# Performance work log

Hardware: AMD Instinct MI355X
Metric: run time of the kernel (lower is better)

Reference implementation:

```python
import jax, jax.numpy as jnp
import numpy as np

NUM_HEADS = 16
MASKED_BIAS = -10000.0


def setup_inputs() -> dict:
    key = jax.random.key(0)
    k1, k2, k3 = jax.random.split(key, 3)
    B, S, D = 4, 2048, 1024
    return {
        "hidden_states": jax.random.normal(k1, (B, S, D), dtype=jnp.float32),
        "attention_mask": jnp.ones((B, S), dtype=jnp.float32),
        "w_attn": jax.random.normal(k2, (D, 3 * D), dtype=jnp.float32) * 0.02,
        "b_attn": jax.random.normal(k3, (3 * D,), dtype=jnp.float32) * 0.1,
    }


def reference(hidden_states, attention_mask, w_attn, b_attn):
    B, S, D = hidden_states.shape
    H = NUM_HEADS
    Dh = D // H
    # Conv1D: x @ W + b  -> [B, S, 3D]
    qkv = hidden_states @ w_attn + b_attn
    q, k, v = jnp.split(qkv, 3, axis=-1)

    def split_heads(t):  # [B,S,D] -> [B,H,S,Dh]
        return t.reshape(B, S, H, Dh).transpose(0, 2, 1, 3)

    q, k, v = split_heads(q), split_heads(k), split_heads(v)
    present = jnp.stack([k, v], axis=0)  # concat_key_value

    # process_mask: (1 - mask) * -10000, broadcast [B,1,1,S]
    add_mask = (1.0 - attention_mask)[:, None, None, :] * MASKED_BIAS

    qk = jnp.einsum("bhqd,bhkd->bhqk", q, k)
    norm_qk = qk * (1.0 / float(Dh) ** 0.5)
    causal = jnp.tril(jnp.ones((S, S), dtype=bool))[None, None]
    attn_weights = jnp.where(causal, norm_qk, jnp.asarray(MASKED_BIAS, norm_qk.dtype))
    attn_weights = attn_weights + add_mask
    probs = jax.nn.softmax(attn_weights, axis=-1)
    attn_output = jnp.einsum("bhqk,bhkd->bhqd", probs, v)
    # merge heads -> [B,S,D]
    attn_output = attn_output.transpose(0, 2, 1, 3).reshape(B, S, D)
    return attn_output, present
```

## Files before the change

kernel.cpp:

```cpp
#include <hip/hip_runtime.h>
#include <stdint.h>


#define B_SZ    4
#define S_LEN   2048
#define D_MODEL 1024
#define N3      3072
#define H_NUM   16
#define DH      64
#define M_TOT   8192

typedef __attribute__((ext_vector_type(8))) short short8;
typedef __attribute__((ext_vector_type(4))) short bf16x4;
typedef __attribute__((ext_vector_type(4))) float f32x4;

#define LOG2E      1.4426950408889634f
#define SCL2E      0.18033688011112042f
#define MASKB2     (-14426.9504f)

__device__ __forceinline__ unsigned short f2b(float f) {
  union { float f; unsigned int u; } x;
  x.f = f;
  unsigned int u = x.u;
  u += 0x7fffu + ((u >> 16) & 1u);
  return (unsigned short)(u >> 16);
}

__device__ __forceinline__ unsigned int cvt_pk_bf16(float lo, float hi) {
  unsigned int r;
  asm("v_cvt_pk_bf16_f32 %0, %1, %2" : "=v"(r) : "v"(lo), "v"(hi));
  return r;
}

__device__ __forceinline__ float exp2_fast(float x) {
#if __has_builtin(__builtin_amdgcn_exp2f)
  return __builtin_amdgcn_exp2f(x);
#else
  return __expf(x * 0.6931471805599453f);
#endif
}

__device__ __forceinline__ f32x4 mfma16(bf16x4 a, bf16x4 b, f32x4 c) {
#if __has_builtin(__builtin_amdgcn_mfma_f32_16x16x16bf16_1k)
  return __builtin_amdgcn_mfma_f32_16x16x16bf16_1k(a, b, c, 0, 0, 0);
#else
  asm("v_mfma_f32_16x16x16_bf16 %0, %1, %2, %0" : "+v"(c) : "v"(a), "v"(b));
  return c;
#endif
}

__device__ __forceinline__ void async16(const void* g, void* l) {
  __builtin_amdgcn_global_load_lds((const __attribute__((address_space(1))) void*)g,
                                   (__attribute__((address_space(3))) void*)l,
                                   16, 0, 0);
}

__global__ void k_convert_x(const float* __restrict__ X, unsigned short* __restrict__ Xb) {
  const int i = (blockIdx.x * 256 + threadIdx.x) * 4;
  const float4 v = *(const float4*)(X + i);
  ushort4 o;
  o.x = f2b(v.x); o.y = f2b(v.y); o.z = f2b(v.z); o.w = f2b(v.w);
  *(ushort4*)(Xb + i) = o;
}

__global__ void k_wt(const float* __restrict__ W, unsigned short* __restrict__ Wt) {
  __shared__ float tile[32][33];
  const int n0 = blockIdx.x * 32, k0 = blockIdx.y * 32;
  const int tx = threadIdx.x, ty = threadIdx.y;
  for (int i = 0; i < 32; i += 8)
    tile[ty + i][tx] = W[(size_t)(k0 + ty + i) * N3 + n0 + tx];
  __syncthreads();
  for (int i = 0; i < 32; i += 8)
    Wt[(size_t)(n0 + ty + i) * D_MODEL + k0 + tx] = f2b(tile[tx][ty + i]);
}

__global__ __launch_bounds__(256) void k_gemm_qkv(
    const unsigned short* __restrict__ Xb, const unsigned short* __restrict__ Wt,
    const float* __restrict__ bias,
    unsigned short* __restrict__ Qb, unsigned short* __restrict__ Kb,
    float* __restrict__ presK, float* __restrict__ presV) {
  __shared__ __align__(16) unsigned short SMEM[8192];
  unsigned short* As = SMEM;
  unsigned short* Bs = SMEM + 4096;
  const int t = threadIdx.x;
  const int lane = t & 63, wave = t >> 6;
  const int g = lane >> 4, c = lane & 15;
  const int m0 = blockIdx.y * 128, n0 = blockIdx.x * 128;
  const int wm = (wave >> 1) * 64, wn = (wave & 1) * 64;

  const f32x4 zero = {0.f, 0.f, 0.f, 0.f};
  f32x4 acc[4][4];
  for (int i = 0; i < 4; ++i)
    for (int j = 0; j < 4; ++j) acc[i][j] = zero;

  const int row_a = t >> 2;
  const int col_a = (t & 3) * 8;
  const unsigned short* gA = Xb + (size_t)(m0 + row_a) * D_MODEL + col_a;
  const unsigned short* gB = Wt + (size_t)(n0 + row_a) * D_MODEL + col_a;
  const int wbase = wave * 1024;

  for (int k0 = 0; k0 < D_MODEL; k0 += 32) {
    __syncthreads();
    async16(gA + k0,                (char*)As + wbase);
    async16(gA + k0 + 64 * D_MODEL, (char*)As + 4096 + wbase);
    async16(gB + k0,                (char*)Bs + wbase);
    async16(gB + k0 + 64 * D_MODEL, (char*)Bs + 4096 + wbase);
    __syncthreads();

    short8 af[4], bf[4];
    for (int mi = 0; mi < 4; ++mi)
      af[mi] = *(const short8*)(As + (wm + mi * 16 + c) * 32 + g * 8);
    for (int ni = 0; ni < 4; ++ni)
      bf[ni] = *(const short8*)(Bs + (wn + ni * 16 + c) * 32 + g * 8);
    for (int mi = 0; mi < 4; ++mi)
      for (int ni = 0; ni < 4; ++ni)
        acc[mi][ni] = __builtin_amdgcn_mfma_f32_16x16x32_bf16(af[mi], bf[ni], acc[mi][ni], 0, 0, 0);
  }

  __syncthreads();

  const int sec = (n0 + wn) >> 10;
  const int h = ((n0 + wn) & 1023) >> 6;
  unsigned short* slab = SMEM + wave * 1152;
  float bv[4];
  for (int ni = 0; ni < 4; ++ni) bv[ni] = bias[n0 + wn + ni * 16 + c];

  for (int mi = 0; mi < 4; ++mi) {
    const int mrow = m0 + wm + mi * 16;

    if (sec != 2) {
      for (int ni = 0; ni < 4; ++ni)
        for (int r = 0; r < 4; ++r)
          slab[(g * 4 + r) * 72 + ni * 16 + c] = f2b(acc[mi][ni][r] + bv[ni]);
      const short8 w0 = *(const short8*)(slab + c * 72 + g * 16);
      const short8 w1 = *(const short8*)(slab + c * 72 + g * 16 + 8);
      const int srow = mrow + c;
      const int b = srow >> 11, s = srow & 2047;
      unsigned short* dst = (sec == 0 ? Qb : Kb) +
          ((size_t)((b * H_NUM + h) * S_LEN + s)) * DH + g * 16;
      *(short8*)(dst) = w0;
      *(short8*)(dst + 8) = w1;
    }
    if (sec >= 1) {
      float* dstf = (sec == 1) ? presK : presV;
      for (int ni = 0; ni < 4; ++ni) {
        const int dh = ni * 16 + c;
        for (int r = 0; r < 4; ++r) {
          const int m = mrow + g * 4 + r;
          const int b = m >> 11, s = m & 2047;
          dstf[((size_t)((b * H_NUM + h) * S_LEN + s)) * DH + dh] =
              acc[mi][ni][r] + bv[ni];
        }
      }
    }
  }
}

__global__ __launch_bounds__(256) void k_vt(const float* __restrict__ presV,
                                            unsigned short* __restrict__ Vt) {
  __shared__ unsigned short tile[64 * 72];
  const int t = threadIdx.x;
  const int bh = blockIdx.y;
  const int s0 = blockIdx.x * 64;
  const int row = t >> 2;
  const int dh0 = (t & 3) * 16;
  const float* src = presV + ((size_t)bh * S_LEN + s0 + row) * DH + dh0;
  for (int i = 0; i < 4; ++i) {
    const float4 v = *(const float4*)(src + i * 4);
    const int dh = dh0 + i * 4;
    tile[(dh + 0) * 72 + row] = f2b(v.x);
    tile[(dh + 1) * 72 + row] = f2b(v.y);
    tile[(dh + 2) * 72 + row] = f2b(v.z);
    tile[(dh + 3) * 72 + row] = f2b(v.w);
  }
  __syncthreads();
  const int dh = t >> 2, p0 = (t & 3) * 16;
  unsigned short* dst = Vt + ((size_t)bh * DH + dh) * S_LEN + s0 + p0;
  short8 o0, o1;
  for (int i = 0; i < 8; ++i) {
    const int pa = p0 + i, pb = p0 + 8 + i;
    const int ka = (((pa >> 2) & 3) << 4) | (((pa >> 4) & 3) << 2) | (pa & 3);
    const int kb = (((pb >> 2) & 3) << 4) | (((pb >> 4) & 3) << 2) | (pb & 3);
    o0[i] = (short)tile[dh * 72 + ka];
    o1[i] = (short)tile[dh * 72 + kb];
  }
  *(short8*)(dst) = o0;
  *(short8*)(dst + 8) = o1;
}

__global__ __launch_bounds__(512) void k_flash(
    const unsigned short* __restrict__ Qb, const unsigned short* __restrict__ Kb,
    const unsigned short* __restrict__ Vt, const float* __restrict__ mask,
    float* __restrict__ out) {
  __shared__ __align__(16) unsigned short Ks[2][64 * 64];
  __shared__ __align__(16) unsigned short Vs[2][64 * 64];
  __shared__ __align__(16) float Ams[S_LEN];
  const int t = threadIdx.x;
  const int lane = t & 63, wave = t >> 6;
  const int g = lane >> 4, c = lane & 15;
  const int bh = blockIdx.y;
  const int b = bh >> 4, h = bh & 15;
  const int srow = t >> 3;
  const int schunk = (t & 7) ^ (srow & 7);
  const unsigned short* gK0 = Kb + ((size_t)bh * S_LEN + srow) * DH + schunk * 8;
  const unsigned short* gV0 = Vt + ((size_t)bh * DH + srow) * S_LEN + schunk * 8;
  const int kslot = c & 7;

  {
    const float4 mv = *(const float4*)(mask + (size_t)b * S_LEN + t * 4);
    float4 o;
    o.x = (1.0f - mv.x) * MASKB2;
    o.y = (1.0f - mv.y) * MASKB2;
    o.z = (1.0f - mv.z) * MASKB2;
    o.w = (1.0f - mv.w) * MASKB2;
    *(float4*)(Ams + t * 4) = o;
  }

  const f32x4 zero = {0.f, 0.f, 0.f, 0.f};

  for (int phase = 0; phase < 2; ++phase) {
    const int x = phase ? 15 - (int)blockIdx.x : (int)blockIdx.x;
    const int qb = x * 128;
    const int qw = qb + wave * 16;
    const int qrow = qw + c;

    short8 bq[2];
    const size_t qoff = ((size_t)bh * S_LEN + qw) * DH;
#pragma unroll
    for (int kc = 0; kc < 2; ++kc)
      bq[kc] = *(const short8*)(Qb + qoff + (size_t)c * DH + kc * 32 + g * 8);

    float m_i = -1e30f, l_i = 0.f;
    f32x4 o_acc[4];
#pragma unroll
    for (int dt = 0; dt < 4; ++dt) o_acc[dt] = zero;

    const int nt = (qb + 128) >> 6;
    async16(gK0, (char*)(&Ks[0][0]) + wave * 1024);
    async16(gV0, (char*)(&Vs[0][0]) + wave * 1024);

    for (int tt = 0; tt < nt; ++tt) {
      const int kb = tt << 6;
      const int cur = tt & 1;
      if (tt + 1 < nt) {
        async16(gK0 + (size_t)(kb + 64) * DH, (char*)(&Ks[cur ^ 1][0]) + wave * 1024);
        async16(gV0 + (kb + 64),              (char*)(&Vs[cur ^ 1][0]) + wave * 1024);
        asm volatile("s_waitcnt vmcnt(2) lgkmcnt(0)" ::: "memory");
      } else {
        asm volatile("s_waitcnt vmcnt(0) lgkmcnt(0)" ::: "memory");
      }
      __builtin_amdgcn_s_barrier();
      __builtin_amdgcn_sched_barrier(0);

      if (qw + 16 > kb) {
        const unsigned short* ks_base = &Ks[cur][0];
        const unsigned short* vs_base = &Vs[cur][0];

        f32x4 sc[4];
#pragma unroll
        for (int ks = 0; ks < 4; ++ks) {
          f32x4 a = zero;
          const int krow = ks * 16 + c;
#pragma unroll
          for (int kc = 0; kc < 2; ++kc) {
            const short8 ak = *(const short8*)(ks_base + krow * 64 + (((kc * 4 + g) ^ kslot) * 8));
            a = __builtin_amdgcn_mfma_f32_16x16x32_bf16(ak, bq[kc], a, 0, 0, 0);
          }
          sc[ks] = a;
        }

        const bool need_causal = (kb + 63 > qw);
        float mxk[4];
#pragma unroll
        for (int ks = 0; ks < 4; ++ks) {
          const float4 amv = *(const float4*)(Ams + kb + ks * 16 + g * 4);
          float am4[4];
          am4[0] = amv.x; am4[1] = amv.y; am4[2] = amv.z; am4[3] = amv.w;
#pragma unroll
          for (int r = 0; r < 4; ++r) {
            float v = sc[ks][r] * SCL2E + am4[r];
            if (need_causal && (kb + ks * 16 + g * 4 + r > qrow))
              v = MASKB2 + am4[r];
            sc[ks][r] = v;
          }
          mxk[ks] = fmaxf(fmaxf(sc[ks][0], sc[ks][1]), fmaxf(sc[ks][2], sc[ks][3]));
        }

        float mx = fmaxf(fmaxf(mxk[0], mxk[1]), fmaxf(mxk[2], mxk[3]));
        mx = fmaxf(mx, __shfl_xor(mx, 16));
        mx = fmaxf(mx, __shfl_xor(mx, 32));
        if (!__all(mx <= m_i + 8.0f)) {
          const float mnew = fmaxf(m_i, mx);
          const float alpha = exp2_fast(m_i - mnew);
          m_i = mnew;
          l_i *= alpha;
#pragma unroll
          for (int dt = 0; dt < 4; ++dt) o_acc[dt] *= alpha;
        }

        bf16x4 pk[4];
        float rsk[4];
#pragma unroll
        for (int ks = 0; ks < 4; ++ks) {
          const float p0 = exp2_fast(sc[ks][0] - m_i);
          const float p1 = exp2_fast(sc[ks][1] - m_i);
          const float p2 = exp2_fast(sc[ks][2] - m_i);
          const float p3 = exp2_fast(sc[ks][3] - m_i);
          rsk[ks] = (p0 + p1) + (p2 + p3);
          union { unsigned int u[2]; bf16x4 v4; } pu;
          pu.u[0] = cvt_pk_bf16(p0, p1);
          pu.u[1] = cvt_pk_bf16(p2, p3);
          pk[ks] = pu.v4;
        }
        float rs = (rsk[0] + rsk[1]) + (rsk[2] + rsk[3]);
        rs += __shfl_xor(rs, 16);
        rs += __shfl_xor(rs, 32);
        l_i += rs;

#pragma unroll
        for (int dt = 0; dt < 4; ++dt) {
          const int vrow = dt * 16 + c;
#pragma unroll
          for (int jp = 0; jp < 2; ++jp) {
            union { short8 s8; bf16x4 h[2]; } vv;
            vv.s8 = *(const short8*)(vs_base + vrow * 64 + (((2 * g + jp) ^ kslot) * 8));
            o_acc[dt] = mfma16(vv.h[0], pk[2 * jp], o_acc[dt]);
            o_acc[dt] = mfma16(vv.h[1], pk[2 * jp + 1], o_acc[dt]);
          }
        }
      }
      __builtin_amdgcn_sched_barrier(0);
      __builtin_amdgcn_s_barrier();
    }

    const float inv = 1.0f / l_i;
    float* orow = out + ((size_t)(b * S_LEN + qrow)) * D_MODEL + h * DH;
#pragma unroll
    for (int dt = 0; dt < 4; ++dt) {
      float4 o;
      o.x = o_acc[dt][0] * inv;
      o.y = o_acc[dt][1] * inv;
      o.z = o_acc[dt][2] * inv;
      o.w = o_acc[dt][3] * inv;
      *(float4*)(orow + dt * 16 + g * 4) = o;
    }
  }
}

extern "C" void kernel_launch(void* const* d_in, const int* in_sizes, int n_in,
                              void* d_out, int out_size, void* d_ws, size_t ws_size,
                              hipStream_t stream) {
  const float* X    = (const float*)d_in[0];
  const float* mask = (const float*)d_in[1];
  const float* W    = (const float*)d_in[2];
  const float* bias = (const float*)d_in[3];

  float* out   = (float*)d_out;
  float* presK = out + (size_t)M_TOT * D_MODEL;
  float* presV = presK + (size_t)M_TOT * D_MODEL;

  char* ws = (char*)d_ws;
  unsigned short* Xb = (unsigned short*)(ws);
  unsigned short* Wt = (unsigned short*)(ws + 16777216);
  unsigned short* Qb = (unsigned short*)(ws + 23068672);
  unsigned short* Kb = (unsigned short*)(ws + 39845888);
  unsigned short* Vt = (unsigned short*)(ws + 56623104);

  k_convert_x<<<dim3(8192), dim3(256), 0, stream>>>(X, Xb);
  k_wt<<<dim3(96, 32), dim3(32, 8), 0, stream>>>(W, Wt);
  k_gemm_qkv<<<dim3(24, 64), dim3(256), 0, stream>>>(Xb, Wt, bias, Qb, Kb, presK, presV);
  k_vt<<<dim3(32, 64), dim3(256), 0, stream>>>(presV, Vt);
  k_flash<<<dim3(8, 64), dim3(512), 0, stream>>>(Qb, Kb, Vt, mask, out);
}
```

Before: 286.2 us.

## Process two query tiles per wave to reuse K/V fragments in flash attention

Each wave now owns 32 query rows, split into two 16-row sub-tiles A and B, so every block covers 256 queries. Each K and V fragment read from LDS feeds two MFMAs instead of one, and the softmax update is factored into a macro applied to each sub-tile. This drops the earlier two-phase scheme that paired query block x with 15-x to balance causal work across blocks, so blocks now carry very unequal amounts of work. The launch bounds also request 4 blocks per CU, which caps registers while the accumulator and score state has doubled, so spilling is a risk.

```diff
diff --git a/kernel.cpp b/kernel.cpp
--- a/kernel.cpp
+++ b/kernel.cpp
@@ -188,7 +188,49 @@
   *(short8*)(dst + 8) = o1;
 }
 
-__global__ __launch_bounds__(512) void k_flash(
+#define SM_TILE(SC, QR, NC, MI, LI, OA, PK)                                 \
+  {                                                                         \
+    float mx = -3.0e38f;                                                    \
+    _Pragma("unroll")                                                       \
+    for (int ks = 0; ks < 4; ++ks) {                                        \
+      _Pragma("unroll")                                                     \
+      for (int r = 0; r < 4; ++r) {                                         \
+        float v = SC[ks][r] * SCL2E + amf[ks][r];                           \
+        if (NC && (kb + ks * 16 + g * 4 + r > (QR))) v = MASKB2 + amf[ks][r];\
+        SC[ks][r] = v;                                                      \
+      }                                                                     \
+      mx = fmaxf(mx, fmaxf(fmaxf(SC[ks][0], SC[ks][1]),                     \
+                           fmaxf(SC[ks][2], SC[ks][3])));                   \
+    }                                                                       \
+    mx = fmaxf(mx, __shfl_xor(mx, 16));                                     \
+    mx = fmaxf(mx, __shfl_xor(mx, 32));                                     \
+    if (!__all(mx <= MI + 8.0f)) {                                          \
+      const float mnew = fmaxf(MI, mx);                                     \
+      const float alpha = exp2_fast(MI - mnew);                             \
+      MI = mnew;                                                            \
+      LI *= alpha;                                                          \
+      _Pragma("unroll")                                                     \
+      for (int dt = 0; dt < 4; ++dt) OA[dt] *= alpha;                       \
+    }                                                                       \
+    float rs = 0.f;                                                         \
+    _Pragma("unroll")                                                       \
+    for (int ks = 0; ks < 4; ++ks) {                                        \
+      const float p0 = exp2_fast(SC[ks][0] - MI);                           \
+      const float p1 = exp2_fast(SC[ks][1] - MI);                           \
+      const float p2 = exp2_fast(SC[ks][2] - MI);                           \
+      const float p3 = exp2_fast(SC[ks][3] - MI);                           \
+      rs += (p0 + p1) + (p2 + p3);                                          \
+      union { unsigned int u[2]; bf16x4 v4; } pu;                           \
+      pu.u[0] = cvt_pk_bf16(p0, p1);                                        \
+      pu.u[1] = cvt_pk_bf16(p2, p3);                                        \
+      PK[ks] = pu.v4;                                                       \
+    }                                                                       \
+    rs += __shfl_xor(rs, 16);                                               \
+    rs += __shfl_xor(rs, 32);                                               \
+    LI += rs;                                                               \
+  }
+
+__global__ __launch_bounds__(512, 4) void k_flash(
     const unsigned short* __restrict__ Qb, const unsigned short* __restrict__ Kb,
     const unsigned short* __restrict__ Vt, const float* __restrict__ mask,
     float* __restrict__ out) {
@@ -218,130 +260,117 @@
 
   const f32x4 zero = {0.f, 0.f, 0.f, 0.f};
 
-  for (int phase = 0; phase < 2; ++phase) {
-    const int x = phase ? 15 - (int)blockIdx.x : (int)blockIdx.x;
-    const int qb = x * 128;
-    const int qw = qb + wave * 16;
-    const int qrow = qw + c;
-
-    short8 bq[2];
+  const int qb = (int)blockIdx.x * 256;
+  const int qw = qb + wave * 32;
+  const int qrA = qw + c;
+  const int qrB = qw + 16 + c;
+
+  short8 bqA[2], bqB[2];
+  {
     const size_t qoff = ((size_t)bh * S_LEN + qw) * DH;
 #pragma unroll
-    for (int kc = 0; kc < 2; ++kc)
-      bq[kc] = *(const short8*)(Qb + qoff + (size_t)c * DH + kc * 32 + g * 8);
-
-    float m_i = -1e30f, l_i = 0.f;
-    f32x4 o_acc[4];
-#pragma unroll
-    for (int dt = 0; dt < 4; ++dt) o_acc[dt] = zero;
-
-    const int nt = (qb + 128) >> 6;
-    async16(gK0, (char*)(&Ks[0][0]) + wave * 1024);
-    async16(gV0, (char*)(&Vs[0][0]) + wave * 1024);
-
-    for (int tt = 0; tt < nt; ++tt) {
-      const int kb = tt << 6;
-      const int cur = tt & 1;
-      if (tt + 1 < nt) {
-        async16(gK0 + (size_t)(kb + 64) * DH, (char*)(&Ks[cur ^ 1][0]) + wave * 1024);
-        async16(gV0 + (kb + 64),              (char*)(&Vs[cur ^ 1][0]) + wave * 1024);
-        asm volatile("s_waitcnt vmcnt(2) lgkmcnt(0)" ::: "memory");
-      } else {
-        asm volatile("s_waitcnt vmcnt(0) lgkmcnt(0)" ::: "memory");
+    for (int kc = 0; kc < 2; ++kc) {
+      bqA[kc] = *(const short8*)(Qb + qoff + (size_t)c * DH + kc * 32 + g * 8);
+      bqB[kc] = *(const short8*)(Qb + qoff + (size_t)(c + 16) * DH + kc * 32 + g * 8);
+    }
+  }
+
+  float m_iA = -1e30f, l_iA = 0.f, m_iB = -1e30f, l_iB = 0.f;
+  f32x4 o_A[4], o_B[4];
+#pragma unroll
+  for (int dt = 0; dt < 4; ++dt) { o_A[dt] = zero; o_B[dt] = zero; }
+
+  const int nt = (qb + 256) >> 6;
+  async16(gK0, (char*)(&Ks[0][0]) + wave * 1024);
+  async16(gV0, (char*)(&Vs[0][0]) + wave * 1024);
+
+  for (int tt = 0; tt < nt; ++tt) {
+    const int kb = tt << 6;
+    const int cur = tt & 1;
+    if (tt + 1 < nt) {
+      async16(gK0 + (size_t)(kb + 64) * DH, (char*)(&Ks[cur ^ 1][0]) + wave * 1024);
+      async16(gV0 + (kb + 64),              (char*)(&Vs[cur ^ 1][0]) + wave * 1024);
+      asm volatile("s_waitcnt vmcnt(2) lgkmcnt(0)" ::: "memory");
+    } else {
+      asm volatile("s_waitcnt vmcnt(0) lgkmcnt(0)" ::: "memory");
+    }
+    __builtin_amdgcn_s_barrier();
+    __builtin_amdgcn_sched_barrier(0);
+
+    if (qw + 32 > kb) {
+      const unsigned short* ks_base = &Ks[cur][0];
+      const unsigned short* vs_base = &Vs[cur][0];
+
+      f32x4 scA[4], scB[4];
+#pragma unroll
+      for (int ks = 0; ks < 4; ++ks) {
+        f32x4 aA = zero, aB = zero;
+        const int krow = ks * 16 + c;
+#pragma unroll
+        for (int kc = 0; kc < 2; ++kc) {
+          const short8 ak = *(const short8*)(ks_base + krow * 64 + (((kc * 4 + g) ^ kslot) * 8));
+          aA = __builtin_amdgcn_mfma_f32_16x16x32_bf16(ak, bqA[kc], aA, 0, 0, 0);
+          aB = __builtin_amdgcn_mfma_f32_16x16x32_bf16(ak, bqB[kc], aB, 0, 0, 0);
+        }
+        scA[ks] = aA;
+        scB[ks] = aB;
       }
-      __builtin_amdgcn_s_barrier();
-      __builtin_amdgcn_sched_barrier(0);
-
-      if (qw + 16 > kb) {
-        const unsigned short* ks_base = &Ks[cur][0];
-        const unsigned short* vs_base = &Vs[cur][0];
-
-        f32x4 sc[4];
-#pragma unroll
-        for (int ks = 0; ks < 4; ++ks) {
-          f32x4 a = zero;
-          const int krow = ks * 16 + c;
-#pragma unroll
-          for (int kc = 0; kc < 2; ++kc) {
-            const short8 ak = *(const short8*)(ks_base + krow * 64 + (((kc * 4 + g) ^ kslot) * 8));
-            a = __builtin_amdgcn_mfma_f32_16x16x32_bf16(ak, bq[kc], a, 0, 0, 0);
-          }
-          sc[ks] = a;
-        }
-
-        const bool need_causal = (kb + 63 > qw);
-        float mxk[4];
-#pragma unroll
-        for (int ks = 0; ks < 4; ++ks) {
-          const float4 amv = *(const float4*)(Ams + kb + ks * 16 + g * 4);
-          float am4[4];
-          am4[0] = amv.x; am4[1] = amv.y; am4[2] = amv.z; am4[3] = amv.w;
-#pragma unroll
-          for (int r = 0; r < 4; ++r) {
-            float v = sc[ks][r] * SCL2E + am4[r];
-            if (need_causal && (kb + ks * 16 + g * 4 + r > qrow))
-              v = MASKB2 + am4[r];
-            sc[ks][r] = v;
-          }
-          mxk[ks] = fmaxf(fmaxf(sc[ks][0], sc[ks][1]), fmaxf(sc[ks][2], sc[ks][3]));
-        }
-
-        float mx = fmaxf(fmaxf(mxk[0], mxk[1]), fmaxf(mxk[2], mxk[3]));
-        mx = fmaxf(mx, __shfl_xor(mx, 16));
-        mx = fmaxf(mx, __shfl_xor(mx, 32));
-        if (!__all(mx <= m_i + 8.0f)) {
-          const float mnew = fmaxf(m_i, mx);
-          const float alpha = exp2_fast(m_i - mnew);
-          m_i = mnew;
-          l_i *= alpha;
-#pragma unroll
-          for (int dt = 0; dt < 4; ++dt) o_acc[dt] *= alpha;
-        }
-
-        bf16x4 pk[4];
-        float rsk[4];
-#pragma unroll
-        for (int ks = 0; ks < 4; ++ks) {
-          const float p0 = exp2_fast(sc[ks][0] - m_i);
-          const float p1 = exp2_fast(sc[ks][1] - m_i);
-          const float p2 = exp2_fast(sc[ks][2] - m_i);
-          const float p3 = exp2_fast(sc[ks][3] - m_i);
-          rsk[ks] = (p0 + p1) + (p2 + p3);
-          union { unsigned int u[2]; bf16x4 v4; } pu;
-          pu.u[0] = cvt_pk_bf16(p0, p1);
-          pu.u[1] = cvt_pk_bf16(p2, p3);
-          pk[ks] = pu.v4;
-        }
-        float rs = (rsk[0] + rsk[1]) + (rsk[2] + rsk[3]);
-        rs += __shfl_xor(rs, 16);
-        rs += __shfl_xor(rs, 32);
-        l_i += rs;
-
-#pragma unroll
-        for (int dt = 0; dt < 4; ++dt) {
-          const int vrow = dt * 16 + c;
-#pragma unroll
-          for (int jp = 0; jp < 2; ++jp) {
-            union { short8 s8; bf16x4 h[2]; } vv;
-            vv.s8 = *(const short8*)(vs_base + vrow * 64 + (((2 * g + jp) ^ kslot) * 8));
-            o_acc[dt] = mfma16(vv.h[0], pk[2 * jp], o_acc[dt]);
-            o_acc[dt] = mfma16(vv.h[1], pk[2 * jp + 1], o_acc[dt]);
-          }
+
+      float amf[4][4];
+#pragma unroll
+      for (int ks = 0; ks < 4; ++ks) {
+        const float4 amv = *(const float4*)(Ams + kb + ks * 16 + g * 4);
+        amf[ks][0] = amv.x; amf[ks][1] = amv.y;
+        amf[ks][2] = amv.z; amf[ks][3] = amv.w;
+      }
+      const bool ncA = (kb + 63 > qw);
+      const bool ncB = (kb + 63 > qw + 16);
+
+      bf16x4 pkA[4], pkB[4];
+      SM_TILE(scA, qrA, ncA, m_iA, l_iA, o_A, pkA)
+      SM_TILE(scB, qrB, ncB, m_iB, l_iB, o_B, pkB)
+
+#pragma unroll
+      for (int dt = 0; dt < 4; ++dt) {
+        const int vrow = dt * 16 + c;
+#pragma unroll
+        for (int jp = 0; jp < 2; ++jp) {
+          union { short8 s8; bf16x4 h[2]; } vv;
+          vv.s8 = *(const short8*)(vs_base + vrow * 64 + (((2 * g + jp) ^ kslot) * 8));
+          o_A[dt] = mfma16(vv.h[0], pkA[2 * jp], o_A[dt]);
+          o_A[dt] = mfma16(vv.h[1], pkA[2 * jp + 1], o_A[dt]);
+          o_B[dt] = mfma16(vv.h[0], pkB[2 * jp], o_B[dt]);
+          o_B[dt] = mfma16(vv.h[1], pkB[2 * jp + 1], o_B[dt]);
         }
       }
-      __builtin_amdgcn_sched_barrier(0);
-      __builtin_amdgcn_s_barrier();
-    }
-
-    const float inv = 1.0f / l_i;
-    float* orow = out + ((size_t)(b * S_LEN + qrow)) * D_MODEL + h * DH;
+    }
+    __builtin_amdgcn_sched_barrier(0);
+    __builtin_amdgcn_s_barrier();
+  }
+
+  {
+    const float inv = 1.0f / l_iA;
+    float* orow = out + ((size_t)(b * S_LEN + qrA)) * D_MODEL + h * DH;
 #pragma unroll
     for (int dt = 0; dt < 4; ++dt) {
       float4 o;
-      o.x = o_acc[dt][0] * inv;
-      o.y = o_acc[dt][1] * inv;
-      o.z = o_acc[dt][2] * inv;
-      o.w = o_acc[dt][3] * inv;
+      o.x = o_A[dt][0] * inv;
+      o.y = o_A[dt][1] * inv;
+      o.z = o_A[dt][2] * inv;
+      o.w = o_A[dt][3] * inv;
+      *(float4*)(orow + dt * 16 + g * 4) = o;
+    }
+  }
+  {
+    const float inv = 1.0f / l_iB;
+    float* orow = out + ((size_t)(b * S_LEN + qrB)) * D_MODEL + h * DH;
+#pragma unroll
+    for (int dt = 0; dt < 4; ++dt) {
+      float4 o;
+      o.x = o_B[dt][0] * inv;
+      o.y = o_B[dt][1] * inv;
+      o.z = o_B[dt][2] * inv;
+      o.w = o_B[dt][3] * inv;
       *(float4*)(orow + dt * 16 + g * 4) = o;
     }
   }
```

After: 352.2 us. 23.1% more time.

## Merge prep kernels and fuse V transpose into QKV GEMM epilogue

Applied to the files above, without the earlier changes.

Combines the X conversion and W transpose kernels into a single launch split by block index, and removes the separate V-transpose kernel by having the GEMM epilogue write bf16 V in the transposed, permuted layout that the flash kernel expects. This removes one launch and a full re-read of fp32 presV from global memory. The trade-off is extra scattered 16-byte stores in the GEMM epilogue, plus a reliance on the MFMA accumulator lane layout matching the old permutation in k_vt.

```diff
diff --git a/kernel.cpp b/kernel.cpp
--- a/kernel.cpp
+++ b/kernel.cpp
@@ -55,30 +55,36 @@
                                    16, 0, 0);
 }
 
-__global__ void k_convert_x(const float* __restrict__ X, unsigned short* __restrict__ Xb) {
-  const int i = (blockIdx.x * 256 + threadIdx.x) * 4;
-  const float4 v = *(const float4*)(X + i);
-  ushort4 o;
-  o.x = f2b(v.x); o.y = f2b(v.y); o.z = f2b(v.z); o.w = f2b(v.w);
-  *(ushort4*)(Xb + i) = o;
-}
-
-__global__ void k_wt(const float* __restrict__ W, unsigned short* __restrict__ Wt) {
+__global__ __launch_bounds__(256) void k_prep(const float* __restrict__ X,
+                                              unsigned short* __restrict__ Xb,
+                                              const float* __restrict__ W,
+                                              unsigned short* __restrict__ Wt) {
   __shared__ float tile[32][33];
-  const int n0 = blockIdx.x * 32, k0 = blockIdx.y * 32;
-  const int tx = threadIdx.x, ty = threadIdx.y;
-  for (int i = 0; i < 32; i += 8)
-    tile[ty + i][tx] = W[(size_t)(k0 + ty + i) * N3 + n0 + tx];
-  __syncthreads();
-  for (int i = 0; i < 32; i += 8)
-    Wt[(size_t)(n0 + ty + i) * D_MODEL + k0 + tx] = f2b(tile[tx][ty + i]);
+  const int bx = blockIdx.x, t = threadIdx.x;
+  if (bx < 8192) {
+    const int i = (bx * 256 + t) * 4;
+    const float4 v = *(const float4*)(X + i);
+    ushort4 o;
+    o.x = f2b(v.x); o.y = f2b(v.y); o.z = f2b(v.z); o.w = f2b(v.w);
+    *(ushort4*)(Xb + i) = o;
+  } else {
+    const int idx = bx - 8192;
+    const int n0 = (idx % 96) * 32, k0 = (idx / 96) * 32;
+    const int tx = t & 31, ty = t >> 5;
+    for (int i = 0; i < 32; i += 8)
+      tile[ty + i][tx] = W[(size_t)(k0 + ty + i) * N3 + n0 + tx];
+    __syncthreads();
+    for (int i = 0; i < 32; i += 8)
+      Wt[(size_t)(n0 + ty + i) * D_MODEL + k0 + tx] = f2b(tile[tx][ty + i]);
+  }
 }
 
 __global__ __launch_bounds__(256) void k_gemm_qkv(
     const unsigned short* __restrict__ Xb, const unsigned short* __restrict__ Wt,
     const float* __restrict__ bias,
     unsigned short* __restrict__ Qb, unsigned short* __restrict__ Kb,
-    float* __restrict__ presK, float* __restrict__ presV) {
+    float* __restrict__ presK, float* __restrict__ presV,
+    unsigned short* __restrict__ Vt) {
   __shared__ __align__(16) unsigned short SMEM[8192];
   unsigned short* As = SMEM;
   unsigned short* Bs = SMEM + 4096;
@@ -154,38 +160,23 @@
       }
     }
   }
-}
-
-__global__ __launch_bounds__(256) void k_vt(const float* __restrict__ presV,
-                                            unsigned short* __restrict__ Vt) {
-  __shared__ unsigned short tile[64 * 72];
-  const int t = threadIdx.x;
-  const int bh = blockIdx.y;
-  const int s0 = blockIdx.x * 64;
-  const int row = t >> 2;
-  const int dh0 = (t & 3) * 16;
-  const float* src = presV + ((size_t)bh * S_LEN + s0 + row) * DH + dh0;
-  for (int i = 0; i < 4; ++i) {
-    const float4 v = *(const float4*)(src + i * 4);
-    const int dh = dh0 + i * 4;
-    tile[(dh + 0) * 72 + row] = f2b(v.x);
-    tile[(dh + 1) * 72 + row] = f2b(v.y);
-    tile[(dh + 2) * 72 + row] = f2b(v.z);
-    tile[(dh + 3) * 72 + row] = f2b(v.w);
-  }
-  __syncthreads();
-  const int dh = t >> 2, p0 = (t & 3) * 16;
-  unsigned short* dst = Vt + ((size_t)bh * DH + dh) * S_LEN + s0 + p0;
-  short8 o0, o1;
-  for (int i = 0; i < 8; ++i) {
-    const int pa = p0 + i, pb = p0 + 8 + i;
-    const int ka = (((pa >> 2) & 3) << 4) | (((pa >> 4) & 3) << 2) | (pa & 3);
-    const int kb = (((pb >> 2) & 3) << 4) | (((pb >> 4) & 3) << 2) | (pb & 3);
-    o0[i] = (short)tile[dh * 72 + ka];
-    o1[i] = (short)tile[dh * 72 + kb];
-  }
-  *(short8*)(dst) = o0;
-  *(short8*)(dst + 8) = o1;
+
+  if (sec == 2) {
+    const int b = (m0 + wm) >> 11, s0 = (m0 + wm) & 2047;
+    for (int ni = 0; ni < 4; ++ni) {
+      const int dh = ni * 16 + c;
+      union { unsigned int u[8]; short8 s8[2]; } pk;
+#pragma unroll
+      for (int mi = 0; mi < 4; ++mi) {
+        pk.u[2 * mi]     = cvt_pk_bf16(acc[mi][ni][0] + bv[ni], acc[mi][ni][1] + bv[ni]);
+        pk.u[2 * mi + 1] = cvt_pk_bf16(acc[mi][ni][2] + bv[ni], acc[mi][ni][3] + bv[ni]);
+      }
+      unsigned short* dst = Vt +
+          ((size_t)((b * H_NUM + h)) * DH + dh) * S_LEN + s0 + g * 16;
+      *(short8*)(dst) = pk.s8[0];
+      *(short8*)(dst + 8) = pk.s8[1];
+    }
+  }
 }
 
 __global__ __launch_bounds__(512) void k_flash(
@@ -322,10 +313,10 @@
           const int vrow = dt * 16 + c;
 #pragma unroll
           for (int jp = 0; jp < 2; ++jp) {
-            union { short8 s8; bf16x4 h[2]; } vv;
+            union { short8 s8; bf16x4 hh[2]; } vv;
             vv.s8 = *(const short8*)(vs_base + vrow * 64 + (((2 * g + jp) ^ kslot) * 8));
-            o_acc[dt] = mfma16(vv.h[0], pk[2 * jp], o_acc[dt]);
-            o_acc[dt] = mfma16(vv.h[1], pk[2 * jp + 1], o_acc[dt]);
+            o_acc[dt] = mfma16(vv.hh[0], pk[2 * jp], o_acc[dt]);
+            o_acc[dt] = mfma16(vv.hh[1], pk[2 * jp + 1], o_acc[dt]);
           }
         }
       }
@@ -366,9 +357,7 @@
   unsigned short* Kb = (unsigned short*)(ws + 39845888);
   unsigned short* Vt = (unsigned short*)(ws + 56623104);
 
-  k_convert_x<<<dim3(8192), dim3(256), 0, stream>>>(X, Xb);
-  k_wt<<<dim3(96, 32), dim3(32, 8), 0, stream>>>(W, Wt);
-  k_gemm_qkv<<<dim3(24, 64), dim3(256), 0, stream>>>(Xb, Wt, bias, Qb, Kb, presK, presV);
-  k_vt<<<dim3(32, 64), dim3(256), 0, stream>>>(presV, Vt);
+  k_prep<<<dim3(11264), dim3(256), 0, stream>>>(X, Xb, W, Wt);
+  k_gemm_qkv<<<dim3(24, 64), dim3(256), 0, stream>>>(Xb, Wt, bias, Qb, Kb, presK, presV, Vt);
   k_flash<<<dim3(8, 64), dim3(512), 0, stream>>>(Qb, Kb, Vt, mask, out);
 }
```

Result: faster. 273.5 us (-4.4%).
